# Kernel tuning notes

Hardware: AMD Instinct MI355X
Metric: run time of the kernel (lower is better)

## Reference

```python
import jax, jax.numpy as jnp
import numpy as np

N_NODES = 100000
N_EDGES = 3200000
N_GRAPHS = 512


def setup_inputs() -> dict:
    key = jax.random.key(0)
    k1, k2, k3, k4, k5 = jax.random.split(key, 5)
    x = jax.random.normal(k1, (N_NODES, 5), dtype=jnp.float32)
    edge_index = jax.random.randint(k2, (2, N_EDGES), 0, N_NODES, dtype=jnp.int64)
    batch = jnp.sort(jax.random.randint(k3, (N_NODES,), 0, N_GRAPHS, dtype=jnp.int64))
    W1 = jax.random.normal(k4, (5, 16), dtype=jnp.float32) * (1.0 / np.sqrt(5.0))
    b1 = jnp.zeros((16,), dtype=jnp.float32)
    W2 = jax.random.normal(k5, (16, 16), dtype=jnp.float32) * 0.25
    b2 = jnp.zeros((16,), dtype=jnp.float32)
    return {"x": x, "edge_index": edge_index, "batch": batch,
            "W1": W1, "b1": b1, "W2": W2, "b2": b2}


def _gcn_conv(x, src, dst, norm, W, b, n_nodes):
    # PyG GCNConv: h = X W; out_i = sum_{j->i} norm_ij * h_j + b
    h = x @ W                                   # [N, out]
    msgs = h[src] * norm[:, None]               # gather + scale  [E_tot, out]
    out = jax.ops.segment_sum(msgs, dst, num_segments=n_nodes)
    return out + b


def reference(x, edge_index, batch, W1, b1, W2, b2):
    n = x.shape[0]
    # add self-loops (GCNConv default)
    loops = jnp.arange(n, dtype=edge_index.dtype)
    src = jnp.concatenate([edge_index[0], loops])
    dst = jnp.concatenate([edge_index[1], loops])
    # symmetric normalization: deg computed on destination nodes
    deg = jax.ops.segment_sum(jnp.ones_like(src, dtype=x.dtype), dst, num_segments=n)
    dinv = jnp.where(deg > 0, jax.lax.rsqrt(deg), 0.0)
    norm = dinv[src] * dinv[dst]                # [E_tot]

    h = jax.nn.relu(_gcn_conv(x, src, dst, norm, W1, b1, n))
    h = jax.nn.relu(_gcn_conv(h, src, dst, norm, W2, b2, n))

    # global mean pool over graphs in the batch
    sums = jax.ops.segment_sum(h, batch, num_segments=N_GRAPHS)
    cnts = jax.ops.segment_sum(jnp.ones((n,), dtype=h.dtype), batch, num_segments=N_GRAPHS)
    return sums / jnp.maximum(cnts, 1.0)[:, None]
```

## Files before the change

kernel.cpp:

```cpp
#include <hip/hip_runtime.h>

#define N_NODES  100000
#define N_EDGES  3200000
#define N_GRAPHS 512
#define F_IN     5
#define F_HID    16

#define PBLK   512
#define CHUNK  8192
#define NCHUNK ((N_EDGES + CHUNK - 1) / CHUNK)
#define BKT_NODES 256
#define NBKT ((N_NODES + BKT_NODES - 1) / BKT_NODES)
#define CAP 10240


__device__ inline unsigned short f2bf(float f) {
    unsigned u = __float_as_uint(f);
    return (unsigned short)((u + 0x7fffu + ((u >> 16) & 1u)) >> 16);
}
__device__ inline float bf2f(unsigned short h) {
    return __uint_as_float(((unsigned)h) << 16);
}
__device__ inline float4 cvt4(ushort4 u) {
    return make_float4(bf2f(u.x), bf2f(u.y), bf2f(u.z), bf2f(u.w));
}
__device__ inline float4 shfl_xor4(float4 v, int m) {
    return make_float4(__shfl_xor(v.x, m, 64), __shfl_xor(v.y, m, 64),
                       __shfl_xor(v.z, m, 64), __shfl_xor(v.w, m, 64));
}

template <int NW>
__device__ inline int block_incl_scan(int v, int t, int* wsum) {
    int lane = t & 63, wave = t >> 6;
    int x = v;
#pragma unroll
    for (int o = 1; o < 64; o <<= 1) {
        int y = __shfl_up(x, o, 64);
        if (lane >= o) x += y;
    }
    if (lane == 63) wsum[wave] = x;
    __syncthreads();
    if (t < 64) {
        int w = (t < NW) ? wsum[t] : 0;
#pragma unroll
        for (int o = 1; o < NW; o <<= 1) {
            int y = __shfl_up(w, o, 64);
            if (t >= o) w += y;
        }
        if (t < NW) wsum[t] = w;
    }
    __syncthreads();
    return x + (wave ? wsum[wave - 1] : 0);
}

__device__ inline float4 row_gather8(const ushort4* __restrict__ pb4, int i, int j,
                                     int beg, int len, const int* __restrict__ col) {
    float4 acc = cvt4(pb4[i * 4 + j]);
    for (int k = 0; k < len; k += 8) {
        int4 c0 = *(const int4*)(col + beg + k);
        int4 c1 = *(const int4*)(col + beg + k + 4);
        ushort4 a0 = pb4[c0.x * 4 + j], a1 = pb4[c0.y * 4 + j];
        ushort4 a2 = pb4[c0.z * 4 + j], a3 = pb4[c0.w * 4 + j];
        ushort4 a4 = pb4[c1.x * 4 + j], a5 = pb4[c1.y * 4 + j];
        ushort4 a6 = pb4[c1.z * 4 + j], a7 = pb4[c1.w * 4 + j];
        float4 f0 = cvt4(a0), f1 = cvt4(a1), f2 = cvt4(a2), f3 = cvt4(a3);
        float4 f4 = cvt4(a4), f5 = cvt4(a5), f6 = cvt4(a6), f7 = cvt4(a7);
        acc.x += ((f0.x + f1.x) + (f2.x + f3.x)) + ((f4.x + f5.x) + (f6.x + f7.x));
        acc.y += ((f0.y + f1.y) + (f2.y + f3.y)) + ((f4.y + f5.y) + (f6.y + f7.y));
        acc.z += ((f0.z + f1.z) + (f2.z + f3.z)) + ((f4.z + f5.z) + (f6.z + f7.z));
        acc.w += ((f0.w + f1.w) + (f2.w + f3.w)) + ((f4.w + f5.w) + (f6.w + f7.w));
    }
    return acc;
}


__global__ void k_zero(int* __restrict__ cursor, float* __restrict__ out,
                       float* __restrict__ cnt, unsigned short* __restrict__ pb_a,
                       unsigned short* __restrict__ pb_b) {
    int i = blockIdx.x * blockDim.x + threadIdx.x;
    if (i < NBKT) cursor[i] = 0;
    if (i < N_GRAPHS * F_HID) out[i] = 0.0f;
    if (i < N_GRAPHS) cnt[i] = 0.0f;
    if (i < F_HID) {
        pb_a[(size_t)N_NODES * F_HID + i] = 0;
        pb_b[(size_t)N_NODES * F_HID + i] = 0;
    }
}

__global__ __launch_bounds__(PBLK) void k_part(const int* __restrict__ src,
                                               const int* __restrict__ dst,
                                               int* __restrict__ cursor,
                                               unsigned* __restrict__ packed) {
    __shared__ int hist[PBLK];
    __shared__ int scn[PBLK];
    __shared__ int rnk[PBLK];
    __shared__ int gbase[PBLK];
    __shared__ int wsum[8];
    int t = threadIdx.x;
    int chunk0 = blockIdx.x * CHUNK;
    int n = min(CHUNK, N_EDGES - chunk0);
    hist[t] = 0;
    __syncthreads();
    int ls[CHUNK / PBLK], ld[CHUNK / PBLK];
    for (int k = t, idx = 0; k < n; k += PBLK, idx++) {
        ls[idx] = src[chunk0 + k];
        ld[idx] = dst[chunk0 + k];
        atomicAdd(&hist[ld[idx] >> 8], 1);
    }
    __syncthreads();
    int v = hist[t];
    int incl = block_incl_scan<8>(v, t, wsum);
    int excl = incl - v;
    scn[t] = excl;
    rnk[t] = excl;
    gbase[t] = (v > 0) ? atomicAdd(&cursor[t], v) : 0;
    __syncthreads();
    for (int k = t, idx = 0; k < n; k += PBLK, idx++) {
        int d = ld[idx], s = ls[idx];
        int b = d >> 8;
        int r = atomicAdd(&rnk[b], 1);
        int g = gbase[b] + (r - scn[b]);
        if (g < CAP)
            packed[(size_t)b * CAP + g] = ((unsigned)s << 8) | (unsigned)(d & 255);
    }
}

__global__ __launch_bounds__(512) void k_csr(const int* __restrict__ cursor,
                                             const unsigned* __restrict__ packed,
                                             const float* __restrict__ x,
                                             const float* __restrict__ W1,
                                             int2* __restrict__ rowbc,
                                             int* __restrict__ col,
                                             float* __restrict__ dinv,
                                             unsigned short* __restrict__ pb) {
    __shared__ int hist[BKT_NODES];
    __shared__ int rnk[BKT_NODES];
    __shared__ int wsum[8];
    __shared__ float w1[F_IN * F_HID];
    int b = blockIdx.x, t = threadIdx.x;
    int n = min(cursor[b], CAP);
    int base = b * CAP;
    if (t < BKT_NODES) hist[t] = 0;
    if (t >= 512 - F_IN * F_HID) w1[t - (512 - F_IN * F_HID)] = W1[t - (512 - F_IN * F_HID)];
    __syncthreads();
    const unsigned* pk = packed + (size_t)b * CAP;
    for (int k = t; k < n; k += 512)
        atomicAdd(&hist[pk[k] & 255], 1);
    __syncthreads();
    int v = (t < BKT_NODES) ? hist[t] : 0;
    int len = (v + 7) & ~7;
    int incl = block_incl_scan<8>(len, t, wsum);
    int excl = incl - len;
    if (t < BKT_NODES) rnk[t] = excl;
    __syncthreads();
    for (int k = t; k < n; k += 512) {
        unsigned w = pk[k];
        int r = atomicAdd(&rnk[w & 255], 1);
        if (r < CAP) col[base + r] = (int)(w >> 8);
    }
    if (t < BKT_NODES) {
        int node = b * BKT_NODES + t;
        if (node < N_NODES) {
            int mylen = min(len, ((CAP - min(excl, CAP)) & ~7));
            for (int q = v; q < mylen; q++) {
                int r = excl + q;
                if (r < CAP) col[base + r] = N_NODES;
            }
            rowbc[node] = make_int2(base + excl, mylen);
            float di = rsqrtf((float)(1 + v));
            dinv[node] = di;
            float xi[F_IN];
#pragma unroll
            for (int k = 0; k < F_IN; k++) xi[k] = x[node * F_IN + k];
            float hv[F_HID];
#pragma unroll
            for (int c = 0; c < F_HID; c++) {
                float h = 0.0f;
#pragma unroll
                for (int k = 0; k < F_IN; k++) h += xi[k] * w1[k * F_HID + c];
                hv[c] = h * di;
            }
            unsigned pkk[8];
#pragma unroll
            for (int q = 0; q < 8; q++)
                pkk[q] = (unsigned)f2bf(hv[2 * q]) | ((unsigned)f2bf(hv[2 * q + 1]) << 16);
            uint4* d4 = (uint4*)(pb + (size_t)node * F_HID);
            d4[0] = make_uint4(pkk[0], pkk[1], pkk[2], pkk[3]);
            d4[1] = make_uint4(pkk[4], pkk[5], pkk[6], pkk[7]);
        }
    }
}

__global__ __launch_bounds__(256) void k_pull_mid(const int2* __restrict__ rowbc,
                                                  const int* __restrict__ col,
                                                  const unsigned short* __restrict__ pb,
                                                  const float* __restrict__ dinv,
                                                  const float* __restrict__ W2,
                                                  const float* __restrict__ b1,
                                                  unsigned short* __restrict__ pb2) {
    __shared__ float w[F_HID * F_HID];
    __shared__ float bb[F_HID];
    int t = threadIdx.x;
    w[t] = W2[t];
    if (t < F_HID) bb[t] = b1[t];
    __syncthreads();
    int gid = blockIdx.x * 256 + t;
    int i = gid >> 2;
    int j = gid & 3;
    if (i >= N_NODES) return;
    int2 rc = rowbc[i];
    float4 acc = row_gather8((const ushort4*)pb, i, j, rc.x, rc.y, col);
    float di = dinv[i];
    float4 mine;
    mine.x = fmaxf(di * acc.x + bb[4 * j + 0], 0.0f);
    mine.y = fmaxf(di * acc.y + bb[4 * j + 1], 0.0f);
    mine.z = fmaxf(di * acc.z + bb[4 * j + 2], 0.0f);
    mine.w = fmaxf(di * acc.w + bb[4 * j + 3], 0.0f);
    float4 o1 = shfl_xor4(mine, 1);
    float4 o2 = shfl_xor4(mine, 2);
    float4 o3 = shfl_xor4(mine, 3);
    float4 hq0 = (j == 0) ? mine : ((j == 1) ? o1 : ((j == 2) ? o2 : o3));
    float4 hq1 = (j == 1) ? mine : ((j == 0) ? o1 : ((j == 3) ? o2 : o3));
    float4 hq2 = (j == 2) ? mine : ((j == 3) ? o1 : ((j == 0) ? o2 : o3));
    float4 hq3 = (j == 3) ? mine : ((j == 2) ? o1 : ((j == 1) ? o2 : o3));
    float hc[F_HID] = {hq0.x, hq0.y, hq0.z, hq0.w, hq1.x, hq1.y, hq1.z, hq1.w,
                       hq2.x, hq2.y, hq2.z, hq2.w, hq3.x, hq3.y, hq3.z, hq3.w};
    float m0 = 0.0f, m1 = 0.0f, m2 = 0.0f, m3 = 0.0f;
#pragma unroll
    for (int c = 0; c < F_HID; c++) {
        float4 wv = *(const float4*)&w[c * F_HID + 4 * j];
        float hv = hc[c];
        m0 += hv * wv.x; m1 += hv * wv.y; m2 += hv * wv.z; m3 += hv * wv.w;
    }
    unsigned p0 = (unsigned)f2bf(m0 * di) | ((unsigned)f2bf(m1 * di) << 16);
    unsigned p1 = (unsigned)f2bf(m2 * di) | ((unsigned)f2bf(m3 * di) << 16);
    *(uint2*)(pb2 + (size_t)i * F_HID + 4 * j) = make_uint2(p0, p1);
}

__global__ __launch_bounds__(256) void k_pull_pool(const int2* __restrict__ rowbc,
                                                   const int* __restrict__ col,
                                                   const unsigned short* __restrict__ pb,
                                                   const float* __restrict__ dinv,
                                                   const int* __restrict__ batch,
                                                   const float* __restrict__ b2,
                                                   float* __restrict__ out,
                                                   float* __restrict__ cnt) {
    __shared__ float bb[F_HID];
    __shared__ float acc2[8][F_HID];
    __shared__ int gcnt[8];
    __shared__ int g0s;
    int t = threadIdx.x;
    if (t < F_HID) bb[t] = b2[t];
    if (t < 8) gcnt[t] = 0;
    if (t < 8 * F_HID) ((float*)acc2)[t] = 0.0f;
    int blk0node = blockIdx.x * 64;
    if (t == 0) g0s = batch[blk0node < N_NODES ? blk0node : N_NODES - 1];
    __syncthreads();
    int g0 = g0s;
    int gid = blockIdx.x * 256 + t;
    int i = gid >> 2;
    int j = gid & 3;
    if (i < N_NODES) {
        int2 rc = rowbc[i];
        float4 acc = row_gather8((const ushort4*)pb, i, j, rc.x, rc.y, col);
        float di = dinv[i];
        float h0 = fmaxf(di * acc.x + bb[4 * j + 0], 0.0f);
        float h1 = fmaxf(di * acc.y + bb[4 * j + 1], 0.0f);
        float h2 = fmaxf(di * acc.z + bb[4 * j + 2], 0.0f);
        float h3 = fmaxf(di * acc.w + bb[4 * j + 3], 0.0f);
        int g = batch[i];
        int l = g - g0;
        if (l >= 0 && l < 8) {
            atomicAdd(&acc2[l][4 * j + 0], h0);
            atomicAdd(&acc2[l][4 * j + 1], h1);
            atomicAdd(&acc2[l][4 * j + 2], h2);
            atomicAdd(&acc2[l][4 * j + 3], h3);
            if (j == 0) atomicAdd(&gcnt[l], 1);
        } else {
            atomicAdd(&out[g * F_HID + 4 * j + 0], h0);
            atomicAdd(&out[g * F_HID + 4 * j + 1], h1);
            atomicAdd(&out[g * F_HID + 4 * j + 2], h2);
            atomicAdd(&out[g * F_HID + 4 * j + 3], h3);
            if (j == 0) atomicAdd(&cnt[g], 1.0f);
        }
    }
    __syncthreads();
    if (t < 8 * F_HID) {
        int l = t >> 4, c = t & 15;
        if (gcnt[l] > 0) atomicAdd(&out[(g0 + l) * F_HID + c], acc2[l][c]);
    }
    if (t < 8 && gcnt[t] > 0) atomicAdd(&cnt[g0 + t], (float)gcnt[t]);
}

__global__ void k_div(float* __restrict__ out, const float* __restrict__ cnt) {
    int i = blockIdx.x * blockDim.x + threadIdx.x;
    if (i < N_GRAPHS * F_HID) {
        float c = cnt[i / F_HID];
        out[i] /= fmaxf(c, 1.0f);
    }
}


extern "C" void kernel_launch(void* const* d_in, const int* in_sizes, int n_in,
                              void* d_out, int out_size, void* d_ws, size_t ws_size,
                              hipStream_t stream) {
    const float* x     = (const float*)d_in[0];
    const int*   ei    = (const int*)d_in[1];
    const int*   batch = (const int*)d_in[2];
    const float* W1    = (const float*)d_in[3];
    const float* b1    = (const float*)d_in[4];
    const float* W2    = (const float*)d_in[5];
    const float* b2    = (const float*)d_in[6];
    float* out = (float*)d_out;

    int*            cursor = (int*)d_ws;
    unsigned*       packed = (unsigned*)(cursor + 512);
    int2*           rowbc  = (int2*)(packed + (size_t)NBKT * CAP);
    int*            col    = (int*)(rowbc + N_NODES);
    float*          dinv   = (float*)(col + (size_t)NBKT * CAP);
    unsigned short* pb_a   = (unsigned short*)(dinv + N_NODES);
    unsigned short* pb_b   = pb_a + (size_t)(N_NODES + 1) * F_HID;
    float*          cnt    = (float*)(pb_b + (size_t)(N_NODES + 1) * F_HID);

    const int* src = ei;
    const int* dst = ei + N_EDGES;

    const int nb_pull = (N_NODES * 4 + 255) / 256;

    k_zero<<<(N_GRAPHS * F_HID + 255) / 256, 256, 0, stream>>>(cursor, out, cnt,
                                                               pb_a, pb_b);
    k_part<<<NCHUNK, PBLK, 0, stream>>>(src, dst, cursor, packed);
    k_csr<<<NBKT, 512, 0, stream>>>(cursor, packed, x, W1, rowbc, col, dinv, pb_a);
    k_pull_mid<<<nb_pull, 256, 0, stream>>>(rowbc, col, pb_a, dinv, W2, b1, pb_b);
    k_pull_pool<<<nb_pull, 256, 0, stream>>>(rowbc, col, pb_b, dinv, batch, b2,
                                             out, cnt);
    k_div<<<(N_GRAPHS * F_HID + 255) / 256, 256, 0, stream>>>(out, cnt);
}
```

Measured before the change: 200.4 us.

## Shard partition cursors, split row gathers across two lanes, fold mean-divide into pool

Bucket cursors are split into 8 shards, selected by chunk index, so the global atomicAdd contention on each bucket cursor in the partition kernel drops. k_csr then walks the shards in turn. The pull kernels assign 8 threads per node, with two halves each taking alternate groups of 8 neighbors and combining via a shuffle, which doubles parallelism for the latency-bound gathers. Per-graph counts are now computed early in k_part so pooling can scale by 1/count directly, removing the k_div launch. Risks: the per-shard capacity of 1280 could overflow for skewed buckets, and k_part's batch-counting covers only blk*256 nodes, so it relies on NCHUNK*256 >= N_NODES.

```diff
diff --git a/kernel.cpp b/kernel.cpp
--- a/kernel.cpp
+++ b/kernel.cpp
@@ -11,7 +11,9 @@
 #define NCHUNK ((N_EDGES + CHUNK - 1) / CHUNK)
 #define BKT_NODES 256
 #define NBKT ((N_NODES + BKT_NODES - 1) / BKT_NODES)
-#define CAP 10240
+#define SHARDS 8
+#define CAP_S  1280
+#define CAP    (SHARDS * CAP_S)
 
 
 __device__ inline unsigned short f2bf(float f) {
@@ -53,10 +55,12 @@
     return x + (wave ? wsum[wave - 1] : 0);
 }
 
-__device__ inline float4 row_gather8(const ushort4* __restrict__ pb4, int i, int j,
-                                     int beg, int len, const int* __restrict__ col) {
-    float4 acc = cvt4(pb4[i * 4 + j]);
-    for (int k = 0; k < len; k += 8) {
+__device__ inline float4 row_gather8s(const ushort4* __restrict__ pb4, int i, int j,
+                                      int half, int beg, int len,
+                                      const int* __restrict__ col) {
+    float4 acc = half ? make_float4(0.f, 0.f, 0.f, 0.f)
+                      : cvt4(pb4[i * 4 + j]);
+    for (int k = half * 8; k < len; k += 16) {
         int4 c0 = *(const int4*)(col + beg + k);
         int4 c1 = *(const int4*)(col + beg + k + 4);
         ushort4 a0 = pb4[c0.x * 4 + j], a1 = pb4[c0.y * 4 + j];
@@ -78,7 +82,7 @@
                        float* __restrict__ cnt, unsigned short* __restrict__ pb_a,
                        unsigned short* __restrict__ pb_b) {
     int i = blockIdx.x * blockDim.x + threadIdx.x;
-    if (i < NBKT) cursor[i] = 0;
+    if (i < NBKT * SHARDS) cursor[i] = 0;
     if (i < N_GRAPHS * F_HID) out[i] = 0.0f;
     if (i < N_GRAPHS) cnt[i] = 0.0f;
     if (i < F_HID) {
@@ -89,17 +93,28 @@
 
 __global__ __launch_bounds__(PBLK) void k_part(const int* __restrict__ src,
                                                const int* __restrict__ dst,
+                                               const int* __restrict__ batch,
                                                int* __restrict__ cursor,
-                                               unsigned* __restrict__ packed) {
+                                               unsigned* __restrict__ packed,
+                                               float* __restrict__ cnt) {
     __shared__ int hist[PBLK];
     __shared__ int scn[PBLK];
     __shared__ int rnk[PBLK];
     __shared__ int gbase[PBLK];
     __shared__ int wsum[8];
+    __shared__ int bcnt[8];
+    __shared__ int g0s;
     int t = threadIdx.x;
-    int chunk0 = blockIdx.x * CHUNK;
+    int blk = blockIdx.x;
+    int s = blk & (SHARDS - 1);
+    int chunk0 = blk * CHUNK;
     int n = min(CHUNK, N_EDGES - chunk0);
     hist[t] = 0;
+    if (t < 8) bcnt[t] = 0;
+    if (t == 0) {
+        int nb = blk * BKT_NODES;
+        g0s = batch[nb < N_NODES ? nb : N_NODES - 1];
+    }
     __syncthreads();
     int ls[CHUNK / PBLK], ld[CHUNK / PBLK];
     for (int k = t, idx = 0; k < n; k += PBLK, idx++) {
@@ -107,21 +122,32 @@
         ld[idx] = dst[chunk0 + k];
         atomicAdd(&hist[ld[idx] >> 8], 1);
     }
+    if (t < BKT_NODES) {
+        int i2 = blk * BKT_NODES + t;
+        if (i2 < N_NODES) {
+            int g = batch[i2];
+            int l = g - g0s;
+            if (l >= 0 && l < 8) atomicAdd(&bcnt[l], 1);
+            else atomicAdd(&cnt[g], 1.0f);
+        }
+    }
     __syncthreads();
     int v = hist[t];
     int incl = block_incl_scan<8>(v, t, wsum);
     int excl = incl - v;
     scn[t] = excl;
     rnk[t] = excl;
-    gbase[t] = (v > 0) ? atomicAdd(&cursor[t], v) : 0;
+    gbase[t] = (v > 0) ? atomicAdd(&cursor[t * SHARDS + s], v) : 0;
+    if (t < 8 && bcnt[t] > 0) atomicAdd(&cnt[g0s + t], (float)bcnt[t]);
     __syncthreads();
     for (int k = t, idx = 0; k < n; k += PBLK, idx++) {
-        int d = ld[idx], s = ls[idx];
+        int d = ld[idx], sr = ls[idx];
         int b = d >> 8;
         int r = atomicAdd(&rnk[b], 1);
         int g = gbase[b] + (r - scn[b]);
-        if (g < CAP)
-            packed[(size_t)b * CAP + g] = ((unsigned)s << 8) | (unsigned)(d & 255);
+        if (g < CAP_S)
+            packed[(size_t)b * CAP + s * CAP_S + g] =
+                ((unsigned)sr << 8) | (unsigned)(d & 255);
     }
 }
 
@@ -136,16 +162,22 @@
     __shared__ int hist[BKT_NODES];
     __shared__ int rnk[BKT_NODES];
     __shared__ int wsum[8];
+    __shared__ int ns[SHARDS];
     __shared__ float w1[F_IN * F_HID];
     int b = blockIdx.x, t = threadIdx.x;
-    int n = min(cursor[b], CAP);
     int base = b * CAP;
     if (t < BKT_NODES) hist[t] = 0;
+    if (t < SHARDS) ns[t] = min(cursor[b * SHARDS + t], CAP_S);
     if (t >= 512 - F_IN * F_HID) w1[t - (512 - F_IN * F_HID)] = W1[t - (512 - F_IN * F_HID)];
     __syncthreads();
     const unsigned* pk = packed + (size_t)b * CAP;
-    for (int k = t; k < n; k += 512)
-        atomicAdd(&hist[pk[k] & 255], 1);
+#pragma unroll
+    for (int s = 0; s < SHARDS; s++) {
+        int m = ns[s];
+        const unsigned* pks = pk + s * CAP_S;
+        for (int k = t; k < m; k += 512)
+            atomicAdd(&hist[pks[k] & 255], 1);
+    }
     __syncthreads();
     int v = (t < BKT_NODES) ? hist[t] : 0;
     int len = (v + 7) & ~7;
@@ -153,10 +185,15 @@
     int excl = incl - len;
     if (t < BKT_NODES) rnk[t] = excl;
     __syncthreads();
-    for (int k = t; k < n; k += 512) {
-        unsigned w = pk[k];
-        int r = atomicAdd(&rnk[w & 255], 1);
-        if (r < CAP) col[base + r] = (int)(w >> 8);
+#pragma unroll
+    for (int s = 0; s < SHARDS; s++) {
+        int m = ns[s];
+        const unsigned* pks = pk + s * CAP_S;
+        for (int k = t; k < m; k += 512) {
+            unsigned w = pks[k];
+            int r = atomicAdd(&rnk[w & 255], 1);
+            if (r < CAP) col[base + r] = (int)(w >> 8);
+        }
     }
     if (t < BKT_NODES) {
         int node = b * BKT_NODES + t;
@@ -205,11 +242,15 @@
     if (t < F_HID) bb[t] = b1[t];
     __syncthreads();
     int gid = blockIdx.x * 256 + t;
-    int i = gid >> 2;
+    int i = gid >> 3;
+    int half = (gid >> 2) & 1;
     int j = gid & 3;
-    if (i >= N_NODES) return;
     int2 rc = rowbc[i];
-    float4 acc = row_gather8((const ushort4*)pb, i, j, rc.x, rc.y, col);
+    float4 acc = row_gather8s((const ushort4*)pb, i, j, half, rc.x, rc.y, col);
+    acc.x += __shfl_xor(acc.x, 4, 64);
+    acc.y += __shfl_xor(acc.y, 4, 64);
+    acc.z += __shfl_xor(acc.z, 4, 64);
+    acc.w += __shfl_xor(acc.w, 4, 64);
     float di = dinv[i];
     float4 mine;
     mine.x = fmaxf(di * acc.x + bb[4 * j + 0], 0.0f);
@@ -232,9 +273,11 @@
         float hv = hc[c];
         m0 += hv * wv.x; m1 += hv * wv.y; m2 += hv * wv.z; m3 += hv * wv.w;
     }
-    unsigned p0 = (unsigned)f2bf(m0 * di) | ((unsigned)f2bf(m1 * di) << 16);
-    unsigned p1 = (unsigned)f2bf(m2 * di) | ((unsigned)f2bf(m3 * di) << 16);
-    *(uint2*)(pb2 + (size_t)i * F_HID + 4 * j) = make_uint2(p0, p1);
+    if (half == 0) {
+        unsigned p0 = (unsigned)f2bf(m0 * di) | ((unsigned)f2bf(m1 * di) << 16);
+        unsigned p1 = (unsigned)f2bf(m2 * di) | ((unsigned)f2bf(m3 * di) << 16);
+        *(uint2*)(pb2 + (size_t)i * F_HID + 4 * j) = make_uint2(p0, p1);
+    }
 }
 
 __global__ __launch_bounds__(256) void k_pull_pool(const int2* __restrict__ rowbc,
@@ -243,8 +286,8 @@
                                                    const float* __restrict__ dinv,
                                                    const int* __restrict__ batch,
                                                    const float* __restrict__ b2,
-                                                   float* __restrict__ out,
-                                                   float* __restrict__ cnt) {
+                                                   const float* __restrict__ cnt,
+                                                   float* __restrict__ out) {
     __shared__ float bb[F_HID];
     __shared__ float acc2[8][F_HID];
     __shared__ int gcnt[8];
@@ -253,16 +296,21 @@
     if (t < F_HID) bb[t] = b2[t];
     if (t < 8) gcnt[t] = 0;
     if (t < 8 * F_HID) ((float*)acc2)[t] = 0.0f;
-    int blk0node = blockIdx.x * 64;
+    int blk0node = blockIdx.x * 32;
     if (t == 0) g0s = batch[blk0node < N_NODES ? blk0node : N_NODES - 1];
     __syncthreads();
     int g0 = g0s;
     int gid = blockIdx.x * 256 + t;
-    int i = gid >> 2;
+    int i = gid >> 3;
+    int half = (gid >> 2) & 1;
     int j = gid & 3;
-    if (i < N_NODES) {
-        int2 rc = rowbc[i];
-        float4 acc = row_gather8((const ushort4*)pb, i, j, rc.x, rc.y, col);
+    int2 rc = rowbc[i];
+    float4 acc = row_gather8s((const ushort4*)pb, i, j, half, rc.x, rc.y, col);
+    acc.x += __shfl_xor(acc.x, 4, 64);
+    acc.y += __shfl_xor(acc.y, 4, 64);
+    acc.z += __shfl_xor(acc.z, 4, 64);
+    acc.w += __shfl_xor(acc.w, 4, 64);
+    if (half == 0) {
         float di = dinv[i];
         float h0 = fmaxf(di * acc.x + bb[4 * j + 0], 0.0f);
         float h1 = fmaxf(di * acc.y + bb[4 * j + 1], 0.0f);
@@ -277,26 +325,20 @@
             atomicAdd(&acc2[l][4 * j + 3], h3);
             if (j == 0) atomicAdd(&gcnt[l], 1);
         } else {
-            atomicAdd(&out[g * F_HID + 4 * j + 0], h0);
-            atomicAdd(&out[g * F_HID + 4 * j + 1], h1);
-            atomicAdd(&out[g * F_HID + 4 * j + 2], h2);
-            atomicAdd(&out[g * F_HID + 4 * j + 3], h3);
-            if (j == 0) atomicAdd(&cnt[g], 1.0f);
+            float inv = 1.0f / cnt[g];
+            atomicAdd(&out[g * F_HID + 4 * j + 0], h0 * inv);
+            atomicAdd(&out[g * F_HID + 4 * j + 1], h1 * inv);
+            atomicAdd(&out[g * F_HID + 4 * j + 2], h2 * inv);
+            atomicAdd(&out[g * F_HID + 4 * j + 3], h3 * inv);
         }
     }
     __syncthreads();
     if (t < 8 * F_HID) {
         int l = t >> 4, c = t & 15;
-        if (gcnt[l] > 0) atomicAdd(&out[(g0 + l) * F_HID + c], acc2[l][c]);
-    }
-    if (t < 8 && gcnt[t] > 0) atomicAdd(&cnt[g0 + t], (float)gcnt[t]);
-}
-
-__global__ void k_div(float* __restrict__ out, const float* __restrict__ cnt) {
-    int i = blockIdx.x * blockDim.x + threadIdx.x;
-    if (i < N_GRAPHS * F_HID) {
-        float c = cnt[i / F_HID];
-        out[i] /= fmaxf(c, 1.0f);
+        if (gcnt[l] > 0) {
+            float inv = 1.0f / cnt[g0 + l];
+            atomicAdd(&out[(g0 + l) * F_HID + c], acc2[l][c] * inv);
+        }
     }
 }
 
@@ -314,7 +356,7 @@
     float* out = (float*)d_out;
 
     int*            cursor = (int*)d_ws;
-    unsigned*       packed = (unsigned*)(cursor + 512);
+    unsigned*       packed = (unsigned*)(cursor + 3200);
     int2*           rowbc  = (int2*)(packed + (size_t)NBKT * CAP);
     int*            col    = (int*)(rowbc + N_NODES);
     float*          dinv   = (float*)(col + (size_t)NBKT * CAP);
@@ -325,14 +367,13 @@
     const int* src = ei;
     const int* dst = ei + N_EDGES;
 
-    const int nb_pull = (N_NODES * 4 + 255) / 256;
+    const int nb_pull = (N_NODES * 8) / 256;
 
     k_zero<<<(N_GRAPHS * F_HID + 255) / 256, 256, 0, stream>>>(cursor, out, cnt,
                                                                pb_a, pb_b);
-    k_part<<<NCHUNK, PBLK, 0, stream>>>(src, dst, cursor, packed);
+    k_part<<<NCHUNK, PBLK, 0, stream>>>(src, dst, batch, cursor, packed, cnt);
     k_csr<<<NBKT, 512, 0, stream>>>(cursor, packed, x, W1, rowbc, col, dinv, pb_a);
     k_pull_mid<<<nb_pull, 256, 0, stream>>>(rowbc, col, pb_a, dinv, W2, b1, pb_b);
     k_pull_pool<<<nb_pull, 256, 0, stream>>>(rowbc, col, pb_b, dinv, batch, b2,
-                                             out, cnt);
-    k_div<<<(N_GRAPHS * F_HID + 255) / 256, 256, 0, stream>>>(out, cnt);
-}
+                                             cnt, out);
+}
```

Result: faster. 189.8 us (-5.3%).
